# Kernel tuning notes

Measured on AMD Instinct MI355X. Metric: run time of the kernel, lower is better.

Reference implementation:

```python
import jax, jax.numpy as jnp
import numpy as np

ACT_BIT = 3
W_BIT = 2


def fake_quant(x, bits):
    """Symmetric uniform fake-quantization to `bits` bits (dequantized values)."""
    qmax = float((1 << (bits - 1)) - 1)
    scale = jnp.max(jnp.abs(x)) / qmax
    scale = jnp.where(scale == 0, jnp.ones_like(scale), scale)
    return jnp.clip(jnp.round(x / scale), -qmax, qmax) * scale


def setup_inputs() -> dict:
    key = jax.random.key(0)
    kA, kX, kWi, kWo = jax.random.split(key, 4)
    N, D_IN, D_H, D_OUT = 8192, 128, 64, 16
    A = jax.random.normal(kA, (N, N), dtype=jnp.float32)       # dense subgraph adjacency (binarized inside)
    X = jax.random.normal(kX, (N, D_IN), dtype=jnp.float32)    # node features
    W_in = jax.random.normal(kWi, (D_IN, D_H), dtype=jnp.float32)
    W_out = jax.random.normal(kWo, (D_H, D_OUT), dtype=jnp.float32)
    return {"A": A, "X": X, "W_in": W_in, "W_out": W_out}


def reference(A, X, W_in, W_out):
    # QGTC GCNConv_Qnt: A quantized to 1 bit, activations to act_bit, weights to w_bit.
    Aq = (A > 0).astype(A.dtype)                 # 1-bit adjacency (bit_qnt(A, 1))
    Xq = fake_quant(X, ACT_BIT)                  # X_Qnt
    Wi = fake_quant(W_in, W_BIT)                 # weight_Qnt
    Wo = fake_quant(W_out, W_BIT)
    # Layer 1: mm_v1(X, W_in) then mm_v1(A, .) with output re-quantized to act_bit
    h = Aq @ (Xq @ Wi)                           # [N, D_H]
    hq = fake_quant(h, ACT_BIT)
    # Layer 2 (output layer)
    out = Aq @ (hq @ Wo)                         # [N, D_OUT]
    return out
```

## Files before the change

### kernel.cpp

```cpp
#include <hip/hip_runtime.h>

#define NN 8192
#define DIN 128
#define DH 64
#define DOUT 16
#define KS 16

typedef _Float16 half8 __attribute__((ext_vector_type(8)));
typedef float f32x4 __attribute__((ext_vector_type(4)));

#define OFF_PART  0u
#define OFF_PART2 2048u
#define OFF_YB    65536u
#define OFF_RT    1114112u
#define OFF_HF    1376256u
#define OFF_BITS  3473408u
#define OFF_P1    11862016u

__device__ __forceinline__ int permk(int k) {
  int e = k & 255;
  return (k & ~255) | (((e & 3) << 6) | (e >> 2));
}

__device__ __forceinline__ float guard(float s) { return (s == 0.0f) ? 1.0f : s; }

__device__ __forceinline__ half8 expand8(unsigned bb) {
  uint4 w;
  w.x = ((bb & 1u)  ? 0x3C00u : 0u) | ((bb & 2u)   ? 0x3C000000u : 0u);
  w.y = ((bb & 4u)  ? 0x3C00u : 0u) | ((bb & 8u)   ? 0x3C000000u : 0u);
  w.z = ((bb & 16u) ? 0x3C00u : 0u) | ((bb & 32u)  ? 0x3C000000u : 0u);
  w.w = ((bb & 64u) ? 0x3C00u : 0u) | ((bb & 128u) ? 0x3C000000u : 0u);
  return __builtin_bit_cast(half8, w);
}

__global__ __launch_bounds__(256) void k_f0(const float* __restrict__ A,
                                            const float* __restrict__ X,
                                            const float* __restrict__ Wi,
                                            const float* __restrict__ Wo,
                                            unsigned char* __restrict__ bits,
                                            unsigned* __restrict__ part) {
  __shared__ float red0[256];
  const int t = threadIdx.x, bid = blockIdx.x;
  const int lane = t & 63, warp = t >> 6;
  for (int c = 0; c < 8; ++c) {
    const size_t wbase = (((size_t)bid * 4 + warp) * 8 + c) * 4096;
    const float4* ap = (const float4*)(A + wbase) + lane;
    unsigned char* bp = bits + (wbase >> 3);
#pragma unroll
    for (int g = 0; g < 16; ++g) {
      float4 v = ap[g * 64];
      unsigned long long m0 = __ballot(v.x > 0.0f);
      unsigned long long m1 = __ballot(v.y > 0.0f);
      unsigned long long m2 = __ballot(v.z > 0.0f);
      unsigned long long m3 = __ballot(v.w > 0.0f);
      unsigned long long lo = (lane & 1) ? m1 : m0;
      unsigned long long hi = (lane & 1) ? m3 : m2;
      unsigned long long word = (lane & 2) ? hi : lo;
      if (lane < 4) *(unsigned long long*)(bp + g * 32 + lane * 8) = word;
    }
  }
  float m = 0.0f;
  if (bid < 240) {
    for (int i = bid * 256 + t; i < NN * DIN; i += 240 * 256) m = fmaxf(m, fabsf(X[i]));
  } else if (bid == 240) {
    for (int i = t; i < DIN * DH; i += 256) m = fmaxf(m, fabsf(Wi[i]));
  } else if (bid == 241) {
    for (int i = t; i < DH * DOUT; i += 256) m = fmaxf(m, fabsf(Wo[i]));
  }
  if (bid < 242) {
    red0[t] = m; __syncthreads();
    for (int s = 128; s > 0; s >>= 1) {
      if (t < s) red0[t] = fmaxf(red0[t], red0[t + s]);
      __syncthreads();
    }
    if (t == 0) part[bid] = __float_as_uint(red0[0]);
  }
}

__global__ __launch_bounds__(256) void k_f1(const float* __restrict__ X,
                                            const float* __restrict__ Wi,
                                            const unsigned* __restrict__ part,
                                            _Float16* __restrict__ Yb) {
  __shared__ float Xs[16][129];
  __shared__ float Ws[DIN][DH];
  __shared__ float red1[256];
  const int t = threadIdx.x, bid = blockIdx.x;
  red1[t] = (t < 240) ? __uint_as_float(part[t]) : 0.0f;
  __syncthreads();
  for (int s = 128; s > 0; s >>= 1) {
    if (t < s) red1[t] = fmaxf(red1[t], red1[t + s]);
    __syncthreads();
  }
  const float sx = guard(red1[0] / 3.0f);
  const float swi = guard(__uint_as_float(part[240]));
  const int k0 = bid * 16;
  for (int i = t; i < 16 * DIN; i += 256) {
    int r = i >> 7, c = i & 127;
    float q = rintf(X[(size_t)(k0 + r) * DIN + c] / sx);
    Xs[r][c] = fminf(fmaxf(q, -3.0f), 3.0f);
  }
  for (int i = t; i < DIN * DH; i += 256) {
    float q = rintf(Wi[i] / swi);
    Ws[i >> 6][i & 63] = fminf(fmaxf(q, -1.0f), 1.0f);
  }
  __syncthreads();
#pragma unroll
  for (int rg = 0; rg < 2; ++rg) {
    const int r = rg * 8 + (t & 7), j = (t >> 3) * 2;
    float a0 = 0.0f, a1 = 0.0f;
    for (int n = 0; n < DIN; ++n) {
      float xv = Xs[r][n];
      a0 = fmaf(xv, Ws[n][j], a0);
      a1 = fmaf(xv, Ws[n][j + 1], a1);
    }
    const int kp = permk(k0 + r);
    const size_t base = (size_t)(kp >> 3) * 512 + (size_t)j * 8 + (kp & 7);
    Yb[base]     = (_Float16)a0;
    Yb[base + 8] = (_Float16)a1;
  }
}

__global__ __launch_bounds__(256) void k_f2(const unsigned char* __restrict__ bits,
                                            const _Float16* __restrict__ Yb,
                                            float* __restrict__ P1) {
  const int t = threadIdx.x, bid = blockIdx.x;
  const int lane = t & 63, warp = t >> 6;
  const int l15 = lane & 15, lq = lane >> 4;
  const int rowblk = bid >> 4, split = bid & 15;
  const int row0 = rowblk * 256 + warp * 64;
  f32x4 acc[4][4] = {};
  const unsigned char* b0 = bits + (size_t)(row0 + l15) * 1024 + split * 64;
#pragma unroll
  for (int it = 0; it < 8; ++it) {
    uint2 w[4];
#pragma unroll
    for (int rt = 0; rt < 4; ++rt)
      w[rt] = *(const uint2*)(b0 + (size_t)rt * 16384 + it * 8);
#pragma unroll
    for (int kk = 0; kk < 2; ++kk) {
      const _Float16* yb = Yb + (size_t)(split * 64 + it * 8 + kk * 4 + lq) * 512 + (size_t)l15 * 8;
      half8 bf[4];
#pragma unroll
      for (int nt = 0; nt < 4; ++nt) bf[nt] = *(const half8*)(yb + nt * 128);
#pragma unroll
      for (int rt = 0; rt < 4; ++rt) {
        half8 af = expand8(((kk ? w[rt].y : w[rt].x) >> (lq * 8)) & 0xffu);
#pragma unroll
        for (int nt = 0; nt < 4; ++nt)
          acc[rt][nt] = __builtin_amdgcn_mfma_f32_16x16x32_f16(af, bf[nt], acc[rt][nt], 0, 0, 0);
      }
    }
  }
  const int r4 = lq * 4;
#pragma unroll
  for (int rt = 0; rt < 4; ++rt)
#pragma unroll
    for (int nt = 0; nt < 4; ++nt)
#pragma unroll
      for (int i = 0; i < 4; ++i)
        P1[((size_t)split * NN + row0 + rt * 16 + r4 + i) * DH + nt * 16 + l15] = acc[rt][nt][i];
}

__global__ __launch_bounds__(256) void k_f3(const float* __restrict__ P1,
                                            float* __restrict__ hf,
                                            unsigned* __restrict__ part2) {
  __shared__ float red3[256];
  const int t = threadIdx.x, bid = blockIdx.x;
  const int idx = bid * 256 + t;
  const float4* p = (const float4*)P1;
  float4 s = {0, 0, 0, 0};
#pragma unroll
  for (int sp = 0; sp < KS; ++sp) {
    float4 v = p[(size_t)sp * (NN * DH / 4) + idx];
    s.x += v.x; s.y += v.y; s.z += v.z; s.w += v.w;
  }
  ((float4*)hf)[idx] = s;
  float m = fmaxf(fmaxf(fabsf(s.x), fabsf(s.y)), fmaxf(fabsf(s.z), fabsf(s.w)));
  red3[t] = m; __syncthreads();
  for (int st = 128; st > 0; st >>= 1) {
    if (t < st) red3[t] = fmaxf(red3[t], red3[t + st]);
    __syncthreads();
  }
  if (t == 0) part2[bid] = __float_as_uint(red3[0]);
}

__global__ __launch_bounds__(256) void k_f4(const float* __restrict__ hf,
                                            const float* __restrict__ Wo,
                                            const unsigned* __restrict__ part,
                                            const unsigned* __restrict__ part2,
                                            _Float16* __restrict__ RT) {
  __shared__ float WoS[DH][DOUT];
  __shared__ float red4[256];
  const int t = threadIdx.x, bid = blockIdx.x;
  red4[t] = fmaxf(__uint_as_float(part2[t]), __uint_as_float(part2[t + 256]));
  __syncthreads();
  for (int s = 128; s > 0; s >>= 1) {
    if (t < s) red4[t] = fmaxf(red4[t], red4[t + s]);
    __syncthreads();
  }
  const float shi = guard(red4[0] / 3.0f);
  const float swo = guard(__uint_as_float(part[241]));
  for (int i = t; i < DH * DOUT; i += 256) {
    float q = rintf(Wo[i] / swo);
    WoS[i >> 4][i & 15] = fminf(fmaxf(q, -1.0f), 1.0f);
  }
  __syncthreads();
  const int i = bid * 16 + (t & 15), j = t >> 4;
  const float4* hp = (const float4*)(hf + (size_t)i * DH);
  float acc = 0.0f;
#pragma unroll 4
  for (int nb = 0; nb < 16; ++nb) {
    float4 h4 = hp[nb];
    float q;
    q = fminf(fmaxf(rintf(h4.x / shi), -3.0f), 3.0f); acc = fmaf(q, WoS[nb * 4 + 0][j], acc);
    q = fminf(fmaxf(rintf(h4.y / shi), -3.0f), 3.0f); acc = fmaf(q, WoS[nb * 4 + 1][j], acc);
    q = fminf(fmaxf(rintf(h4.z / shi), -3.0f), 3.0f); acc = fmaf(q, WoS[nb * 4 + 2][j], acc);
    q = fminf(fmaxf(rintf(h4.w / shi), -3.0f), 3.0f); acc = fmaf(q, WoS[nb * 4 + 3][j], acc);
  }
  RT[(size_t)j * NN + permk(i)] = (_Float16)acc;
}

__global__ __launch_bounds__(256) void k_f5(const unsigned char* __restrict__ bits,
                                            const _Float16* __restrict__ RT,
                                            const unsigned* __restrict__ part,
                                            const unsigned* __restrict__ part2,
                                            float* __restrict__ out) {
  __shared__ float redP[256];
  __shared__ float red2s[3][16][16];
  const int t = threadIdx.x, bid = blockIdx.x;
  redP[t] = (t < 240) ? __uint_as_float(part[t]) : 0.0f;
  __syncthreads();
  for (int s = 128; s > 0; s >>= 1) {
    if (t < s) redP[t] = fmaxf(redP[t], redP[t + s]);
    __syncthreads();
  }
  const float sxraw = redP[0];
  __syncthreads();
  redP[t] = fmaxf(__uint_as_float(part2[t]), __uint_as_float(part2[t + 256]));
  __syncthreads();
  for (int s = 128; s > 0; s >>= 1) {
    if (t < s) redP[t] = fmaxf(redP[t], redP[t + s]);
    __syncthreads();
  }
  const float maxint = redP[0];
  const float swi = guard(__uint_as_float(part[240]));
  const float swo = guard(__uint_as_float(part[241]));
  const float sx = guard(sxraw / 3.0f);
  const float shF = (maxint == 0.0f) ? 1.0f : (sx * swi) * (maxint / 3.0f);
  const float sfin = shF * swo;

  const int lane = t & 63, warp = t >> 6;
  const int l15 = lane & 15, lq = lane >> 4;
  const int row0 = bid * 16;
  const unsigned char* brow = bits + (size_t)(row0 + l15) * 1024 + warp * 256;
  const _Float16* rrow = RT + (size_t)l15 * NN + warp * 2048 + lq * 8;
  f32x4 acc = {};
#pragma unroll 8
  for (int it = 0; it < 32; ++it) {
    uint2 w = *(const uint2*)(brow + it * 8);
#pragma unroll
    for (int kk = 0; kk < 2; ++kk) {
      half8 af = expand8(((kk ? w.y : w.x) >> (lq * 8)) & 0xffu);
      half8 bf = *(const half8*)(rrow + it * 64 + kk * 32);
      acc = __builtin_amdgcn_mfma_f32_16x16x32_f16(af, bf, acc, 0, 0, 0);
    }
  }
  if (warp > 0) {
#pragma unroll
    for (int i = 0; i < 4; ++i) red2s[warp - 1][lq * 4 + i][l15] = acc[i];
  }
  __syncthreads();
  if (warp == 0) {
#pragma unroll
    for (int i = 0; i < 4; ++i) {
      int r = lq * 4 + i;
      float v = acc[i] + red2s[0][r][l15] + red2s[1][r][l15] + red2s[2][r][l15];
      out[(size_t)(row0 + r) * DOUT + l15] = v * sfin;
    }
  }
}

extern "C" void kernel_launch(void* const* d_in, const int* in_sizes, int n_in,
                              void* d_out, int out_size, void* d_ws, size_t ws_size,
                              hipStream_t stream) {
  const float* A  = (const float*)d_in[0];
  const float* X  = (const float*)d_in[1];
  const float* Wi = (const float*)d_in[2];
  const float* Wo = (const float*)d_in[3];
  char* ws = (char*)d_ws;
  unsigned* part      = (unsigned*)(ws + OFF_PART);
  unsigned* part2     = (unsigned*)(ws + OFF_PART2);
  _Float16* Yb        = (_Float16*)(ws + OFF_YB);
  _Float16* RT        = (_Float16*)(ws + OFF_RT);
  float* hf           = (float*)(ws + OFF_HF);
  unsigned char* bits = (unsigned char*)(ws + OFF_BITS);
  float* P1           = (float*)(ws + OFF_P1);
  float* outp         = (float*)d_out;

  k_f0<<<512, 256, 0, stream>>>(A, X, Wi, Wo, bits, part);
  k_f1<<<512, 256, 0, stream>>>(X, Wi, part, Yb);
  k_f2<<<512, 256, 0, stream>>>(bits, Yb, P1);
  k_f3<<<512, 256, 0, stream>>>(P1, hf, part2);
  k_f4<<<512, 256, 0, stream>>>(hf, Wo, part, part2, RT);
  k_f5<<<512, 256, 0, stream>>>(bits, RT, part, part2, outp);
}
```

Baseline: 157.2 us.

## Fuse split-K adjacency GEMM with reduction and re-grid binarize and XW kernels

The split-K layer-1 aggregation and its separate partial-sum reduction kernel are replaced by one kernel. In it, each block covers 64 rows and 4 warps split K, and the partials are reduced in shared memory along with the abs-max. This drops the large P1 round trip through global memory and one launch. The A-binarize kernel is spread over 4096 blocks using nontemporal loads, and the X·W kernel over 1024 blocks. The fused GEMM launches only 128 blocks, which may underfill the GPU and lengthen the per-block K loop.

Measured after the change: 133.1 us. 15.3% less time.

```diff
diff --git a/kernel.cpp b/kernel.cpp
--- a/kernel.cpp
+++ b/kernel.cpp
@@ -4,7 +4,6 @@
 #define DIN 128
 #define DH 64
 #define DOUT 16
-#define KS 16
 
 typedef _Float16 half8 __attribute__((ext_vector_type(8)));
 typedef float f32x4 __attribute__((ext_vector_type(4)));
@@ -15,7 +14,6 @@
 #define OFF_RT    1114112u
 #define OFF_HF    1376256u
 #define OFF_BITS  3473408u
-#define OFF_P1    11862016u
 
 __device__ __forceinline__ int permk(int k) {
   int e = k & 255;
@@ -39,62 +37,63 @@
                                             const float* __restrict__ Wo,
                                             unsigned char* __restrict__ bits,
                                             unsigned* __restrict__ part) {
-  __shared__ float red0[256];
-  const int t = threadIdx.x, bid = blockIdx.x;
-  const int lane = t & 63, warp = t >> 6;
-  for (int c = 0; c < 8; ++c) {
-    const size_t wbase = (((size_t)bid * 4 + warp) * 8 + c) * 4096;
-    const float4* ap = (const float4*)(A + wbase) + lane;
+  const int t = threadIdx.x, bx = blockIdx.x;
+  if (bx < 4096) {
+    const int lane = t & 63, warp = t >> 6;
+    const size_t wbase = ((size_t)bx * 4 + warp) * 4096;
+    const f32x4* ap = (const f32x4*)(A + wbase) + lane;
     unsigned char* bp = bits + (wbase >> 3);
 #pragma unroll
     for (int g = 0; g < 16; ++g) {
-      float4 v = ap[g * 64];
-      unsigned long long m0 = __ballot(v.x > 0.0f);
-      unsigned long long m1 = __ballot(v.y > 0.0f);
-      unsigned long long m2 = __ballot(v.z > 0.0f);
-      unsigned long long m3 = __ballot(v.w > 0.0f);
+      f32x4 v = __builtin_nontemporal_load(&ap[g * 64]);
+      unsigned long long m0 = __ballot(v[0] > 0.0f);
+      unsigned long long m1 = __ballot(v[1] > 0.0f);
+      unsigned long long m2 = __ballot(v[2] > 0.0f);
+      unsigned long long m3 = __ballot(v[3] > 0.0f);
       unsigned long long lo = (lane & 1) ? m1 : m0;
       unsigned long long hi = (lane & 1) ? m3 : m2;
       unsigned long long word = (lane & 2) ? hi : lo;
       if (lane < 4) *(unsigned long long*)(bp + g * 32 + lane * 8) = word;
     }
-  }
+    return;
+  }
+  __shared__ float red[256];
+  const int b = bx - 4096;
   float m = 0.0f;
-  if (bid < 240) {
-    for (int i = bid * 256 + t; i < NN * DIN; i += 240 * 256) m = fmaxf(m, fabsf(X[i]));
-  } else if (bid == 240) {
+  if (b < 240) {
+    for (int i = b * 256 + t; i < NN * DIN; i += 240 * 256) m = fmaxf(m, fabsf(X[i]));
+  } else if (b == 240) {
     for (int i = t; i < DIN * DH; i += 256) m = fmaxf(m, fabsf(Wi[i]));
-  } else if (bid == 241) {
+  } else {
     for (int i = t; i < DH * DOUT; i += 256) m = fmaxf(m, fabsf(Wo[i]));
   }
-  if (bid < 242) {
-    red0[t] = m; __syncthreads();
-    for (int s = 128; s > 0; s >>= 1) {
-      if (t < s) red0[t] = fmaxf(red0[t], red0[t + s]);
-      __syncthreads();
-    }
-    if (t == 0) part[bid] = __float_as_uint(red0[0]);
-  }
+  red[t] = m; __syncthreads();
+  for (int s = 128; s > 0; s >>= 1) {
+    if (t < s) red[t] = fmaxf(red[t], red[t + s]);
+    __syncthreads();
+  }
+  if (t == 0) part[b] = __float_as_uint(red[0]);
 }
 
 __global__ __launch_bounds__(256) void k_f1(const float* __restrict__ X,
                                             const float* __restrict__ Wi,
                                             const unsigned* __restrict__ part,
                                             _Float16* __restrict__ Yb) {
-  __shared__ float Xs[16][129];
+  __shared__ float red[256];
+  __shared__ float Xs[8][129];
   __shared__ float Ws[DIN][DH];
-  __shared__ float red1[256];
-  const int t = threadIdx.x, bid = blockIdx.x;
-  red1[t] = (t < 240) ? __uint_as_float(part[t]) : 0.0f;
-  __syncthreads();
-  for (int s = 128; s > 0; s >>= 1) {
-    if (t < s) red1[t] = fmaxf(red1[t], red1[t + s]);
-    __syncthreads();
-  }
-  const float sx = guard(red1[0] / 3.0f);
+  const int t = threadIdx.x;
+  red[t] = (t < 240) ? __uint_as_float(part[t]) : 0.0f;
+  __syncthreads();
+  for (int s = 128; s > 0; s >>= 1) {
+    if (t < s) red[t] = fmaxf(red[t], red[t + s]);
+    __syncthreads();
+  }
+  const float sx = guard(red[0] / 3.0f);
   const float swi = guard(__uint_as_float(part[240]));
-  const int k0 = bid * 16;
-  for (int i = t; i < 16 * DIN; i += 256) {
+  const int k0 = blockIdx.x * 8;
+  __syncthreads();
+  for (int i = t; i < 8 * DIN; i += 256) {
     int r = i >> 7, c = i & 127;
     float q = rintf(X[(size_t)(k0 + r) * DIN + c] / sx);
     Xs[r][c] = fminf(fmaxf(q, -3.0f), 3.0f);
@@ -104,84 +103,79 @@
     Ws[i >> 6][i & 63] = fminf(fmaxf(q, -1.0f), 1.0f);
   }
   __syncthreads();
-#pragma unroll
-  for (int rg = 0; rg < 2; ++rg) {
-    const int r = rg * 8 + (t & 7), j = (t >> 3) * 2;
-    float a0 = 0.0f, a1 = 0.0f;
-    for (int n = 0; n < DIN; ++n) {
-      float xv = Xs[r][n];
-      a0 = fmaf(xv, Ws[n][j], a0);
-      a1 = fmaf(xv, Ws[n][j + 1], a1);
-    }
-    const int kp = permk(k0 + r);
-    const size_t base = (size_t)(kp >> 3) * 512 + (size_t)j * 8 + (kp & 7);
-    Yb[base]     = (_Float16)a0;
-    Yb[base + 8] = (_Float16)a1;
-  }
-}
-
-__global__ __launch_bounds__(256) void k_f2(const unsigned char* __restrict__ bits,
+  const int r = t & 7, jp = t >> 3, j = jp * 2;
+  float a0 = 0.0f, a1 = 0.0f;
+  for (int n = 0; n < DIN; ++n) {
+    float xv = Xs[r][n];
+    a0 = fmaf(xv, Ws[n][j], a0);
+    a1 = fmaf(xv, Ws[n][j + 1], a1);
+  }
+  const int kp = permk(k0 + r);
+  const size_t base = (size_t)(kp >> 3) * 512 + (size_t)j * 8 + (kp & 7);
+  Yb[base]     = (_Float16)a0;
+  Yb[base + 8] = (_Float16)a1;
+}
+
+__global__ __launch_bounds__(256) void k_g1(const unsigned char* __restrict__ bits,
                                             const _Float16* __restrict__ Yb,
-                                            float* __restrict__ P1) {
-  const int t = threadIdx.x, bid = blockIdx.x;
-  const int lane = t & 63, warp = t >> 6;
-  const int l15 = lane & 15, lq = lane >> 4;
-  const int rowblk = bid >> 4, split = bid & 15;
-  const int row0 = rowblk * 256 + warp * 64;
-  f32x4 acc[4][4] = {};
-  const unsigned char* b0 = bits + (size_t)(row0 + l15) * 1024 + split * 64;
-#pragma unroll
-  for (int it = 0; it < 8; ++it) {
-    uint2 w[4];
-#pragma unroll
-    for (int rt = 0; rt < 4; ++rt)
-      w[rt] = *(const uint2*)(b0 + (size_t)rt * 16384 + it * 8);
-#pragma unroll
-    for (int kk = 0; kk < 2; ++kk) {
-      const _Float16* yb = Yb + (size_t)(split * 64 + it * 8 + kk * 4 + lq) * 512 + (size_t)l15 * 8;
-      half8 bf[4];
-#pragma unroll
-      for (int nt = 0; nt < 4; ++nt) bf[nt] = *(const half8*)(yb + nt * 128);
-#pragma unroll
-      for (int rt = 0; rt < 4; ++rt) {
-        half8 af = expand8(((kk ? w[rt].y : w[rt].x) >> (lq * 8)) & 0xffu);
-#pragma unroll
-        for (int nt = 0; nt < 4; ++nt)
-          acc[rt][nt] = __builtin_amdgcn_mfma_f32_16x16x32_f16(af, bf[nt], acc[rt][nt], 0, 0, 0);
-      }
-    }
-  }
-  const int r4 = lq * 4;
-#pragma unroll
-  for (int rt = 0; rt < 4; ++rt)
-#pragma unroll
-    for (int nt = 0; nt < 4; ++nt)
-#pragma unroll
-      for (int i = 0; i < 4; ++i)
-        P1[((size_t)split * NN + row0 + rt * 16 + r4 + i) * DH + nt * 16 + l15] = acc[rt][nt][i];
-}
-
-__global__ __launch_bounds__(256) void k_f3(const float* __restrict__ P1,
                                             float* __restrict__ hf,
                                             unsigned* __restrict__ part2) {
-  __shared__ float red3[256];
-  const int t = threadIdx.x, bid = blockIdx.x;
-  const int idx = bid * 256 + t;
-  const float4* p = (const float4*)P1;
-  float4 s = {0, 0, 0, 0};
-#pragma unroll
-  for (int sp = 0; sp < KS; ++sp) {
-    float4 v = p[(size_t)sp * (NN * DH / 4) + idx];
-    s.x += v.x; s.y += v.y; s.z += v.z; s.w += v.w;
-  }
-  ((float4*)hf)[idx] = s;
-  float m = fmaxf(fmaxf(fabsf(s.x), fabsf(s.y)), fmaxf(fabsf(s.z), fabsf(s.w)));
-  red3[t] = m; __syncthreads();
-  for (int st = 128; st > 0; st >>= 1) {
-    if (t < st) red3[t] = fmaxf(red3[t], red3[t + st]);
-    __syncthreads();
-  }
-  if (t == 0) part2[bid] = __float_as_uint(red3[0]);
+  __shared__ float hs[3][64][64];
+  const int t = threadIdx.x, lane = t & 63, warp = t >> 6;
+  const int l15 = lane & 15, lq = lane >> 4;
+  const int row0 = blockIdx.x * 64;
+  f32x4 acc[4][4] = {};
+  const unsigned char* b0 = bits + (size_t)(row0 + l15) * 1024 + warp * 256;
+#pragma unroll 4
+  for (int it = 0; it < 32; ++it) {
+    uint2 w[4];
+#pragma unroll
+    for (int mt = 0; mt < 4; ++mt)
+      w[mt] = *(const uint2*)(b0 + (size_t)mt * 16384 + it * 8);
+#pragma unroll
+    for (int kk = 0; kk < 2; ++kk) {
+      const _Float16* yb = Yb + (size_t)(warp * 256 + it * 8 + kk * 4 + lq) * 512 + (size_t)l15 * 8;
+      half8 bf[4];
+#pragma unroll
+      for (int nt = 0; nt < 4; ++nt) bf[nt] = *(const half8*)(yb + nt * 128);
+#pragma unroll
+      for (int mt = 0; mt < 4; ++mt) {
+        half8 af = expand8(((kk ? w[mt].y : w[mt].x) >> (lq * 8)) & 0xffu);
+#pragma unroll
+        for (int nt = 0; nt < 4; ++nt)
+          acc[mt][nt] = __builtin_amdgcn_mfma_f32_16x16x32_f16(af, bf[nt], acc[mt][nt], 0, 0, 0);
+      }
+    }
+  }
+  const int r4 = lq * 4;
+  if (warp > 0) {
+#pragma unroll
+    for (int mt = 0; mt < 4; ++mt)
+#pragma unroll
+      for (int nt = 0; nt < 4; ++nt)
+#pragma unroll
+        for (int i = 0; i < 4; ++i)
+          hs[warp - 1][mt * 16 + r4 + i][nt * 16 + l15] = acc[mt][nt][i];
+  }
+  __syncthreads();
+  if (warp == 0) {
+    float m = 0.0f;
+#pragma unroll
+    for (int mt = 0; mt < 4; ++mt) {
+#pragma unroll
+      for (int nt = 0; nt < 4; ++nt) {
+#pragma unroll
+        for (int i = 0; i < 4; ++i) {
+          const int rr = mt * 16 + r4 + i, cc = nt * 16 + l15;
+          float v = acc[mt][nt][i] + hs[0][rr][cc] + hs[1][rr][cc] + hs[2][rr][cc];
+          hf[(size_t)(row0 + rr) * DH + cc] = v;
+          m = fmaxf(m, fabsf(v));
+        }
+      }
+    }
+    for (int off = 32; off > 0; off >>= 1) m = fmaxf(m, __shfl_xor(m, off));
+    if (t == 0) part2[blockIdx.x] = __float_as_uint(m);
+  }
 }
 
 __global__ __launch_bounds__(256) void k_f4(const float* __restrict__ hf,
@@ -192,7 +186,7 @@
   __shared__ float WoS[DH][DOUT];
   __shared__ float red4[256];
   const int t = threadIdx.x, bid = blockIdx.x;
-  red4[t] = fmaxf(__uint_as_float(part2[t]), __uint_as_float(part2[t + 256]));
+  red4[t] = (t < 128) ? __uint_as_float(part2[t]) : 0.0f;
   __syncthreads();
   for (int s = 128; s > 0; s >>= 1) {
     if (t < s) red4[t] = fmaxf(red4[t], red4[t + s]);
@@ -236,7 +230,7 @@
   }
   const float sxraw = redP[0];
   __syncthreads();
-  redP[t] = fmaxf(__uint_as_float(part2[t]), __uint_as_float(part2[t + 256]));
+  redP[t] = (t < 128) ? __uint_as_float(part2[t]) : 0.0f;
   __syncthreads();
   for (int s = 128; s > 0; s >>= 1) {
     if (t < s) redP[t] = fmaxf(redP[t], redP[t + s]);
@@ -294,13 +288,11 @@
   _Float16* RT        = (_Float16*)(ws + OFF_RT);
   float* hf           = (float*)(ws + OFF_HF);
   unsigned char* bits = (unsigned char*)(ws + OFF_BITS);
-  float* P1           = (float*)(ws + OFF_P1);
   float* outp         = (float*)d_out;
 
-  k_f0<<<512, 256, 0, stream>>>(A, X, Wi, Wo, bits, part);
-  k_f1<<<512, 256, 0, stream>>>(X, Wi, part, Yb);
-  k_f2<<<512, 256, 0, stream>>>(bits, Yb, P1);
-  k_f3<<<512, 256, 0, stream>>>(P1, hf, part2);
+  k_f0<<<4338, 256, 0, stream>>>(A, X, Wi, Wo, bits, part);
+  k_f1<<<1024, 256, 0, stream>>>(X, Wi, part, Yb);
+  k_g1<<<128, 256, 0, stream>>>(bits, Yb, hf, part2);
   k_f4<<<512, 256, 0, stream>>>(hf, Wo, part, part2, RT);
   k_f5<<<512, 256, 0, stream>>>(bits, RT, part, part2, outp);
 }
```
